# Kernel optimization log

Hardware: AMD Instinct MI355X
Metric: run time of the kernel (lower is better)

## Reference

```python
import jax, jax.numpy as jnp
import numpy as np

N, E, G = 50000, 800000, 16
NODE, HID, OUT, HEADS = 128, 64, 128, 3
NEG_SLOPE = 0.2

def setup_inputs() -> dict:
    key = jax.random.key(0)
    ks = jax.random.split(key, 12)
    h = jax.random.normal(ks[0], (N, NODE), jnp.float32)
    z = jax.random.normal(ks[1], (G, OUT), jnp.float32)
    src = jax.random.randint(ks[2], (E,), 0, N, jnp.int32)
    dst = jax.random.randint(ks[3], (E,), 0, N, jnp.int32)
    graph_id = jnp.sort(jax.random.randint(ks[4], (N,), 0, G, jnp.int32))
    s = 0.1
    fc_w = jax.random.normal(ks[5], (HEADS * HID, NODE), jnp.float32) * s
    attn_l = jax.random.normal(ks[6], (HEADS, HID), jnp.float32) * s
    attn_r = jax.random.normal(ks[7], (HEADS, HID), jnp.float32) * s
    bias = jnp.zeros((HEADS * HID,), jnp.float32)
    lin1_w = jax.random.normal(ks[8], (HID, OUT), jnp.float32) * s
    lin1_b = jnp.zeros((HID,), jnp.float32)
    lin2_w = jax.random.normal(ks[9], (1, 2 * HID), jnp.float32) * s
    lin2_b = jnp.zeros((1,), jnp.float32)
    return dict(h=h, z=z, src=src, dst=dst, graph_id=graph_id, fc_w=fc_w,
                attn_l=attn_l, attn_r=attn_r, bias=bias,
                lin1_w=lin1_w, lin1_b=lin1_b, lin2_w=lin2_w, lin2_b=lin2_b)

def reference(h, z, src, dst, graph_id, fc_w, attn_l, attn_r, bias,
              lin1_w, lin1_b, lin2_w, lin2_b):
    n = h.shape[0]
    # GATConv: projection -> [N, H, D]
    feat = (h @ fc_w.T).reshape(n, HEADS, HID)
    el = jnp.sum(feat * attn_l, axis=-1)  # [N, H]
    er = jnp.sum(feat * attn_r, axis=-1)  # [N, H]
    e = jax.nn.leaky_relu(el[src] + er[dst], NEG_SLOPE)  # [E, H]
    # edge softmax per destination node
    m = jax.ops.segment_max(e, dst, num_segments=n)
    e = jnp.exp(e - m[dst])
    s = jax.ops.segment_sum(e, dst, num_segments=n)
    alpha = e / s[dst]
    # scatter-weighted aggregation
    msg = alpha[:, :, None] * feat[src]  # [E, H, D]
    rst = jax.ops.segment_sum(msg, dst, num_segments=n)  # [N, H, D]
    rst = rst + bias.reshape(HEADS, HID)
    h_d = jnp.mean(rst, axis=1)  # [N, D] (mean over heads)
    # dgl.mean_nodes: per-graph mean pooling
    counts = jax.ops.segment_sum(jnp.ones((n,), h_d.dtype), graph_id, num_segments=G)
    pooled = jax.ops.segment_sum(h_d, graph_id, num_segments=G) / jnp.maximum(counts, 1.0)[:, None]
    z1 = z @ lin1_w.T + lin1_b  # [G, HID]
    cat = jnp.concatenate([pooled, z1], axis=1)  # [G, 2*HID]
    score = jax.nn.sigmoid(cat @ lin2_w.T + lin2_b)  # [G, 1]
    return score
```

## Files before the change

kernel.cpp:

```cpp
#include <hip/hip_runtime.h>
#include <math.h>

#define N_NODES 50000
#define N_EDGES 800000
#define N_GRAPHS 16
#define NODE_F 128
#define HID 64
#define OUT_F 128
#define HEADS 3
#define NEG 0.2f
#define FEAT (HEADS*HID)

typedef float f32x4 __attribute__((ext_vector_type(4)));
typedef float f32x2 __attribute__((ext_vector_type(2)));
typedef short bf16x8 __attribute__((ext_vector_type(8)));

#if defined(__has_builtin)
#if __has_builtin(__builtin_amdgcn_cvt_pk_f32_fp8) && __has_builtin(__builtin_amdgcn_cvt_pk_fp8_f32)
#define USE_FP8 1
#endif
#endif
#ifndef USE_FP8
#define USE_FP8 0
#endif

#if USE_FP8
#define FB 1
#else
#define FB 2
#endif
#define GRP (8 * FB)
#define ROW (32 * GRP)

#define DEG_PAD 32

__device__ __forceinline__ ushort f2bf(float x) {
  union { float f; unsigned u; } v; v.f = x;
  unsigned r = v.u + 0x7fff + ((v.u >> 16) & 1);
  return (ushort)(r >> 16);
}
__device__ __forceinline__ float bf2f(ushort x) {
  union { unsigned u; float f; } v; v.u = ((unsigned)x) << 16;
  return v.f;
}

__device__ __forceinline__ void feat_store(unsigned char* base, int n, int hh, int dd, float v) {
  size_t off = (size_t)n * ROW + (dd >> 1) * GRP + ((hh * 2 + (dd & 1)) * FB);
#if USE_FP8
  base[off] = (unsigned char)(__builtin_amdgcn_cvt_pk_fp8_f32(v, 0.f, 0, false) & 0xff);
#else
  *(ushort*)(base + off) = f2bf(v);
#endif
}

#define ZERO_INTS (N_GRAPHS * HID + N_GRAPHS + N_NODES * DEG_PAD)
#define ZERO_U4 (ZERO_INTS / 4)
#define ZB ((ZERO_U4 + 255) / 256)
__global__ void kprep(const float* __restrict__ fc_w, ushort* __restrict__ fcb,
                      uint4* __restrict__ zbase) {
  if (blockIdx.x >= 24) {
    int i = (blockIdx.x - 24) * 256 + threadIdx.x;
    if (i < ZERO_U4) zbase[i] = make_uint4(0, 0, 0, 0);
    return;
  }
  int i = blockIdx.x * 256 + threadIdx.x;
  int col = i >> 5;
  int kb = (i & 31) * 4;
  float4 v = *(const float4*)(fc_w + (size_t)col * NODE_F + kb);
  int t = col >> 4, m = col & 15;
  int kk = kb >> 5, kq = (kb >> 3) & 3, j = kb & 7;
  size_t idx0 = ((((size_t)t * 4 + kk) * 4 + kq) * 16 + m) * 8 + j;
  ushort4 o; o.x = f2bf(v.x); o.y = f2bf(v.y); o.z = f2bf(v.z); o.w = f2bf(v.w);
  *(ushort4*)(fcb + idx0) = o;
}

#define GB0 ((N_NODES + 63) / 64)
#define EB 5
#define HB2 (N_EDGES / (256 * EB))
__global__ __launch_bounds__(256) void k01_fused(
    const float* __restrict__ h, const ushort* __restrict__ fcb,
    const float* __restrict__ attn_l, const float* __restrict__ attn_r,
    const int* __restrict__ dst,
    unsigned char* __restrict__ feat, float* __restrict__ el, float* __restrict__ er,
    int* __restrict__ deg, int* __restrict__ rank)
{
  __shared__ ushort A[64][136];
  const int tid = threadIdx.x;

  if (blockIdx.x < HB2) {
    const int base = blockIdx.x * (256 * EB) + tid;
    int d[EB], r[EB];
#pragma unroll
    for (int i = 0; i < EB; i++) d[i] = dst[base + i * 256];
#pragma unroll
    for (int i = 0; i < EB; i++) r[i] = atomicAdd(&deg[d[i] * DEG_PAD], 1);
#pragma unroll
    for (int i = 0; i < EB; i++) rank[base + i * 256] = r[i];
    return;
  }

  const int n0 = (blockIdx.x - HB2) * 64;
  for (int i = tid; i < 64 * 32; i += 256) {
    int r = i >> 5, c4 = i & 31;
    if (n0 + r < N_NODES) {
      float4 v = *(const float4*)(h + (size_t)(n0 + r) * NODE_F + c4 * 4);
      unsigned lo = f2bf(v.x) | ((unsigned)f2bf(v.y) << 16);
      unsigned hi = f2bf(v.z) | ((unsigned)f2bf(v.w) << 16);
      *(uint2*)&A[r][c4 * 4] = make_uint2(lo, hi);
    }
  }
  __syncthreads();

  const int lane = tid & 63, wv = tid >> 6;
  const int m = lane & 15, kq = lane >> 4;

  f32x4 acc[12];
#pragma unroll
  for (int t = 0; t < 12; t++) acc[t] = (f32x4){0.f, 0.f, 0.f, 0.f};

#pragma unroll
  for (int kk = 0; kk < 4; kk++) {
    bf16x8 af = *(const bf16x8*)&A[wv * 16 + m][kk * 32 + kq * 8];
#pragma unroll
    for (int t = 0; t < 12; t++) {
      const bf16x8 bf = *(const bf16x8*)(fcb + ((((size_t)t * 4 + kk) * 4 + kq) * 16 + m) * 8);
      acc[t] = __builtin_amdgcn_mfma_f32_16x16x32_bf16(af, bf, acc[t], 0, 0, 0);
    }
  }

  const int rbase = n0 + wv * 16 + kq * 4;
#pragma unroll
  for (int t = 0; t < 12; t++) {
    const int hh = t >> 2;
    const int dd = (t & 3) * 16 + m;
#pragma unroll
    for (int reg = 0; reg < 4; reg++) {
      int n = rbase + reg;
      if (n < N_NODES) feat_store(feat, n, hh, dd, acc[t][reg]);
    }
  }

#pragma unroll
  for (int hh = 0; hh < HEADS; hh++) {
    float elv[4] = {0.f, 0.f, 0.f, 0.f};
    float erv[4] = {0.f, 0.f, 0.f, 0.f};
#pragma unroll
    for (int tt = 0; tt < 4; tt++) {
      int t = hh * 4 + tt;
      float al = attn_l[hh * HID + tt * 16 + m];
      float ar = attn_r[hh * HID + tt * 16 + m];
#pragma unroll
      for (int reg = 0; reg < 4; reg++) {
        elv[reg] = fmaf(acc[t][reg], al, elv[reg]);
        erv[reg] = fmaf(acc[t][reg], ar, erv[reg]);
      }
    }
#pragma unroll
    for (int reg = 0; reg < 4; reg++) {
#pragma unroll
      for (int off = 1; off < 16; off <<= 1) {
        elv[reg] += __shfl_xor(elv[reg], off, 64);
        erv[reg] += __shfl_xor(erv[reg], off, 64);
      }
      int n = rbase + reg;
      if (m == 0 && n < N_NODES) {
        el[(size_t)n * 4 + hh] = elv[reg];
        er[(size_t)n * 4 + hh] = erv[reg];
      }
    }
  }
}

#define SCAN_T 1024
#define SCAN_NB 49

__global__ __launch_bounds__(SCAN_T) void k2a_blocksum(
    const int* __restrict__ deg, int* __restrict__ bsum)
{
  const int tid = threadIdx.x;
  int idx = blockIdx.x * SCAN_T + tid;
  int v = (idx < N_NODES) ? deg[(size_t)idx * DEG_PAD] : 0;
#pragma unroll
  for (int off = 32; off; off >>= 1) v += __shfl_xor(v, off, 64);
  __shared__ int ws_[16];
  if ((tid & 63) == 0) ws_[tid >> 6] = v;
  __syncthreads();
  if (tid == 0) {
    int s = 0;
    for (int i = 0; i < 16; i++) s += ws_[i];
    bsum[blockIdx.x] = s;
  }
}

__global__ __launch_bounds__(SCAN_T) void k2c_apply(
    const int* __restrict__ deg, const int* __restrict__ bsum,
    int* __restrict__ offs)
{
  __shared__ int wsum[16], woff[16], bo;
  const int tid = threadIdx.x;
  const int lane = tid & 63, wv = tid >> 6;
  const int idx = blockIdx.x * SCAN_T + tid;
  if (tid < 64) {
    int v = (tid < blockIdx.x) ? bsum[tid] : 0;
#pragma unroll
    for (int off = 32; off; off >>= 1) v += __shfl_xor(v, off, 64);
    if (tid == 0) bo = v;
  }
  int v = (idx < N_NODES) ? deg[(size_t)idx * DEG_PAD] : 0;
  int s = v;
#pragma unroll
  for (int off = 1; off < 64; off <<= 1) {
    int t = __shfl_up(s, off, 64);
    if (lane >= off) s += t;
  }
  if (lane == 63) wsum[wv] = s;
  __syncthreads();
  if (tid < 16) {
    int w = wsum[tid];
    int sc = w;
#pragma unroll
    for (int off = 1; off < 16; off <<= 1) {
      int t = __shfl_up(sc, off, 64);
      if (tid >= off) sc += t;
    }
    woff[tid] = sc - w;
  }
  __syncthreads();
  int excl = s - v + woff[wv] + bo;
  if (idx < N_NODES) offs[idx] = excl;
  if (blockIdx.x == 0 && tid == 0) offs[N_NODES] = N_EDGES;
}

__global__ __launch_bounds__(256) void k3_edge(
    const int* __restrict__ src, const int* __restrict__ dst,
    const float* __restrict__ el4, const float* __restrict__ er4,
    const int* __restrict__ offs, const int* __restrict__ rank,
    float4* __restrict__ csr_w)
{
  int e = blockIdx.x * 256 + threadIdx.x;
  int s = src[e], d = dst[e];
  int pos = offs[d] + rank[e];
  float4 elv = ((const float4*)el4)[s];
  float4 erv = ((const float4*)er4)[d];
  float e0 = elv.x + erv.x; e0 = e0 > 0.f ? e0 : NEG * e0;
  float e1 = elv.y + erv.y; e1 = e1 > 0.f ? e1 : NEG * e1;
  float e2 = elv.z + erv.z; e2 = e2 > 0.f ? e2 : NEG * e2;
  float4 r;
  r.x = __expf(e0); r.y = __expf(e1); r.z = __expf(e2);
  r.w = __int_as_float(s * ROW);
  csr_w[pos] = r;
}

__global__ __launch_bounds__(256) void k4_agg(
    const int* __restrict__ offs, const float4* __restrict__ csr_w,
    const unsigned char* __restrict__ feat, const float* __restrict__ bias,
    float* __restrict__ h_d)
{
  __shared__ float4 rec[4][64];
  const int wv = threadIdx.x >> 6, lane = threadIdx.x & 63;
  const int n = blockIdx.x * 4 + wv;
  const int lo = offs[n], hi = offs[n + 1];
  const int half = lane >> 5;
  const int d = lane & 31;
  const char* fb = (const char*)feat;

  float a0x = 0.f, a0y = 0.f, a1x = 0.f, a1y = 0.f, a2x = 0.f, a2y = 0.f;
  float s0 = 0.f, s1 = 0.f, s2 = 0.f;

  for (int base = lo; base < hi; base += 64) {
    const int cnt = min(64, hi - base);
    if (lane < cnt) {
      float4 c = csr_w[base + lane];
      rec[wv][lane] = c;
      s0 += c.x; s1 += c.y; s2 += c.z;
    }
#define K4_BODY(J) do { \
      float4 c = rec[wv][J]; \
      const char* rp = fb + __float_as_int(c.w) + GRP * d; \
      f32x2 f0, f1, f2; \
      if (USE_FP8) { \
        uint2 q = *(const uint2*)rp; \
        f0 = __builtin_amdgcn_cvt_pk_f32_fp8(q.x & 0xffff, false); \
        f1 = __builtin_amdgcn_cvt_pk_f32_fp8(q.x >> 16, false); \
        f2 = __builtin_amdgcn_cvt_pk_f32_fp8(q.y & 0xffff, false); \
      } else { \
        uint4 q = *(const uint4*)rp; \
        f0.x = bf2f((ushort)(q.x & 0xffff)); f0.y = bf2f((ushort)(q.x >> 16)); \
        f1.x = bf2f((ushort)(q.y & 0xffff)); f1.y = bf2f((ushort)(q.y >> 16)); \
        f2.x = bf2f((ushort)(q.z & 0xffff)); f2.y = bf2f((ushort)(q.z >> 16)); \
      } \
      a0x = fmaf(c.x, f0.x, a0x); a0y = fmaf(c.x, f0.y, a0y); \
      a1x = fmaf(c.y, f1.x, a1x); a1y = fmaf(c.y, f1.y, a1y); \
      a2x = fmaf(c.z, f2.x, a2x); a2y = fmaf(c.z, f2.y, a2y); \
    } while (0)
    int j = half;
    for (; j + 2 < cnt; j += 4) { K4_BODY(j); K4_BODY(j + 2); }
    if (j < cnt) K4_BODY(j);
#undef K4_BODY
  }
  a0x += __shfl_xor(a0x, 32, 64); a0y += __shfl_xor(a0y, 32, 64);
  a1x += __shfl_xor(a1x, 32, 64); a1y += __shfl_xor(a1y, 32, 64);
  a2x += __shfl_xor(a2x, 32, 64); a2y += __shfl_xor(a2y, 32, 64);
#pragma unroll
  for (int off = 32; off; off >>= 1) {
    s0 += __shfl_xor(s0, off, 64);
    s1 += __shfl_xor(s1, off, 64);
    s2 += __shfl_xor(s2, off, 64);
  }
  const float i0 = s0 > 0.f ? 1.f / s0 : 0.f;
  const float i1 = s1 > 0.f ? 1.f / s1 : 0.f;
  const float i2 = s2 > 0.f ? 1.f / s2 : 0.f;
  if (half == 0) {
    float2 b0 = *(const float2*)(bias + 2 * d);
    float2 b1 = *(const float2*)(bias + HID + 2 * d);
    float2 b2 = *(const float2*)(bias + 2 * HID + 2 * d);
    float2 o;
    o.x = (fmaf(a0x, i0, b0.x) + fmaf(a1x, i1, b1.x) + fmaf(a2x, i2, b2.x)) * (1.f / 3.f);
    o.y = (fmaf(a0y, i0, b0.y) + fmaf(a1y, i1, b1.y) + fmaf(a2y, i2, b2.y)) * (1.f / 3.f);
    *(float2*)(h_d + (size_t)n * HID + 2 * d) = o;
  }
}

#define K5_NPB 128
#define K5_NB ((N_NODES + K5_NPB - 1) / K5_NPB)
#define NSEG (K5_NB * 2)
__global__ __launch_bounds__(256) void k5a_partial(
    const int* __restrict__ graph_id, const float* __restrict__ h_d,
    float* __restrict__ pooled_res, int* __restrict__ gcnt_res,
    float* __restrict__ part, int* __restrict__ pg, int* __restrict__ pc)
{
  const int wv = threadIdx.x >> 6, lane = threadIdx.x & 63;
  const int b = blockIdx.x;
  const int n0 = b * K5_NPB;
  const int n1 = min(n0 + K5_NPB, N_NODES);
  const int g_lo = graph_id[n0], g_hi = graph_id[n1 - 1];

  if (g_hi > g_lo + 1) {
    float acc = 0.f; int cur_g = -1; int cnt = 0;
    for (int i = n0 + wv; i < n1; i += 4) {
      int g = graph_id[i];
      if (g != cur_g) {
        if (cur_g >= 0) {
          atomicAdd(&pooled_res[cur_g * HID + lane], acc);
          if (lane == 0) atomicAdd(&gcnt_res[cur_g], cnt);
        }
        acc = 0.f; cnt = 0; cur_g = g;
      }
      acc += h_d[(size_t)i * HID + lane];
      cnt++;
    }
    if (cur_g >= 0) {
      atomicAdd(&pooled_res[cur_g * HID + lane], acc);
      if (lane == 0) atomicAdd(&gcnt_res[cur_g], cnt);
    }
    if (threadIdx.x < 2) pg[b * 2 + threadIdx.x] = -1;
    return;
  }

  float acc_lo = 0.f, acc_hi = 0.f;
  int c_lo = 0, c_hi = 0;
  for (int i = n0 + wv; i < n1; i += 4) {
    int g = graph_id[i];
    float v = h_d[(size_t)i * HID + lane];
    bool hi = (g != g_lo);
    acc_hi += hi ? v : 0.f;
    acc_lo += hi ? 0.f : v;
    c_hi += hi ? 1 : 0;
    c_lo += hi ? 0 : 1;
  }
  __shared__ float ls[2][4][64];
  __shared__ int lc[2][4];
  ls[0][wv][lane] = acc_lo;
  ls[1][wv][lane] = acc_hi;
  if (lane == 0) { lc[0][wv] = c_lo; lc[1][wv] = c_hi; }
  __syncthreads();
  if (wv < 2) {
    float s = ls[wv][0][lane] + ls[wv][1][lane] + ls[wv][2][lane] + ls[wv][3][lane];
    part[((size_t)b * 2 + wv) * HID + lane] = s;
    if (lane == 0) {
      int cnt = lc[wv][0] + lc[wv][1] + lc[wv][2] + lc[wv][3];
      int gg = (wv == 0) ? g_lo : g_hi;
      if (wv == 1 && (g_hi == g_lo || cnt == 0)) gg = -1;
      pg[b * 2 + wv] = gg;
      pc[b * 2 + wv] = cnt;
    }
  }
}

__global__ __launch_bounds__(256) void k6_final(
    const float* __restrict__ part, const int* __restrict__ pg, const int* __restrict__ pc,
    const float* __restrict__ pooled_res, const int* __restrict__ gcnt_res,
    const float* __restrict__ z,
    const float* __restrict__ lin1_w, const float* __restrict__ lin1_b,
    const float* __restrict__ lin2_w, const float* __restrict__ lin2_b,
    float* __restrict__ out)
{
  const int g = blockIdx.x;
  const int tid = threadIdx.x, wv = tid >> 6, lane = tid & 63;
  __shared__ int spg[NSEG], spc[NSEG];
  __shared__ float red[4][HID];
  __shared__ int rc[4];
  __shared__ float cat[2 * HID];

  for (int i = tid; i < NSEG; i += 256) { spg[i] = pg[i]; spc[i] = pc[i]; }
  __syncthreads();

  float acc = 0.f; int cnt = 0;
  for (int s = wv; s < NSEG; s += 4) {
    if (spg[s] == g) {
      acc += part[(size_t)s * HID + lane];
      cnt += spc[s];
    }
  }
  red[wv][lane] = acc;
  if (lane == 0) rc[wv] = cnt;
  __syncthreads();

  if (wv == 0) {
    float s = red[0][lane] + red[1][lane] + red[2][lane] + red[3][lane]
            + pooled_res[g * HID + lane];
    int c = rc[0] + rc[1] + rc[2] + rc[3] + gcnt_res[g];
    cat[lane] = s / (float)(c > 0 ? c : 1);
  }
  if (wv == 1) {
    float s = lin1_b[lane];
    const float* zr = z + g * OUT_F;
    const float* wr = lin1_w + lane * OUT_F;
    for (int k = 0; k < OUT_F; k += 4) {
      float4 zv = *(const float4*)(zr + k);
      float4 wv4 = *(const float4*)(wr + k);
      s = fmaf(zv.x, wv4.x, fmaf(zv.y, wv4.y, fmaf(zv.z, wv4.z, fmaf(zv.w, wv4.w, s))));
    }
    cat[HID + lane] = s;
  }
  __syncthreads();
  if (wv == 0) {
    float s = cat[lane] * lin2_w[lane] + cat[HID + lane] * lin2_w[HID + lane];
#pragma unroll
    for (int off = 32; off; off >>= 1) s += __shfl_xor(s, off, 64);
    if (lane == 0) out[g] = 1.f / (1.f + __expf(-(s + lin2_b[0])));
  }
}

extern "C" void kernel_launch(void* const* d_in, const int* in_sizes, int n_in,
                              void* d_out, int out_size, void* d_ws, size_t ws_size,
                              hipStream_t stream) {
  (void)in_sizes; (void)n_in; (void)out_size; (void)ws_size;
  const float* h      = (const float*)d_in[0];
  const float* z      = (const float*)d_in[1];
  const int*   src    = (const int*)d_in[2];
  const int*   dst    = (const int*)d_in[3];
  const int*   gid    = (const int*)d_in[4];
  const float* fc_w   = (const float*)d_in[5];
  const float* attn_l = (const float*)d_in[6];
  const float* attn_r = (const float*)d_in[7];
  const float* bias   = (const float*)d_in[8];
  const float* lin1_w = (const float*)d_in[9];
  const float* lin1_b = (const float*)d_in[10];
  const float* lin2_w = (const float*)d_in[11];
  const float* lin2_b = (const float*)d_in[12];
  float* out = (float*)d_out;

  float4* csr_w     = (float4*)d_ws;
  unsigned char* feat = (unsigned char*)(csr_w + N_EDGES);
  float* h_d        = (float*)(feat + (size_t)N_NODES * ROW);
  float* el         = h_d + (size_t)N_NODES * HID;
  float* er         = el + (size_t)N_NODES * 4;
  float* part       = er + (size_t)N_NODES * 4;
  int* pg           = (int*)(part + (size_t)NSEG * HID);
  int* pc           = pg + NSEG;
  ushort* fcb       = (ushort*)(pc + NSEG);
  float* pooled_res = (float*)(fcb + 192 * NODE_F);
  int* gcnt_res     = (int*)(pooled_res + N_GRAPHS * HID);
  int* deg          = gcnt_res + N_GRAPHS;
  int* offs         = deg + (size_t)N_NODES * DEG_PAD;
  int* rank         = offs + (N_NODES + 1);
  int* bsum         = rank + N_EDGES;

  kprep<<<24 + ZB, 256, 0, stream>>>(fc_w, fcb, (uint4*)pooled_res);
  k01_fused<<<HB2 + GB0, 256, 0, stream>>>(h, fcb, attn_l, attn_r, dst,
                                           feat, el, er, deg, rank);
  k2a_blocksum<<<SCAN_NB, SCAN_T, 0, stream>>>(deg, bsum);
  k2c_apply<<<SCAN_NB, SCAN_T, 0, stream>>>(deg, bsum, offs);
  k3_edge<<<N_EDGES / 256, 256, 0, stream>>>(src, dst, el, er, offs, rank, csr_w);
  k4_agg<<<N_NODES / 4, 256, 0, stream>>>(offs, csr_w, feat, bias, h_d);
  k5a_partial<<<K5_NB, 256, 0, stream>>>(gid, h_d, pooled_res, gcnt_res, part, pg, pc);
  k6_final<<<N_GRAPHS, 256, 0, stream>>>(part, pg, pc, pooled_res, gcnt_res,
                                         z, lin1_w, lin1_b, lin2_w, lin2_b, out);
}
```

Before: 229.5 us.

## Replace global-atomic CSR build with two-level bucketed counting sort

Replaces the per-edge global atomic degree counting (with padded counters) and two-kernel scan with a two-pass bucketed counting sort. Edges are first histogrammed into 64-node buckets with shared-memory atomics, then scanned and scattered into buckets, and finally sorted per node within each bucket. This removes contended global atomics and the padded degree array, and lets k3_edge read sorted (src,dst) pairs and write output contiguously. In exchange it adds more kernel launches, an extra pass over the edges, and no longer overlaps the GEMM with the degree counting.

```diff
diff --git a/kernel.cpp b/kernel.cpp
--- a/kernel.cpp
+++ b/kernel.cpp
@@ -32,7 +32,9 @@
 #define GRP (8 * FB)
 #define ROW (32 * GRP)
 
-#define DEG_PAD 32
+#define NBKT ((N_NODES + 63) / 64)
+#define H1B 400
+#define EPB (N_EDGES / H1B)
 
 __device__ __forceinline__ ushort f2bf(float x) {
   union { float f; unsigned u; } v; v.f = x;
@@ -53,7 +55,7 @@
 #endif
 }
 
-#define ZERO_INTS (N_GRAPHS * HID + N_GRAPHS + N_NODES * DEG_PAD)
+#define ZERO_INTS (N_GRAPHS * HID + N_GRAPHS)
 #define ZERO_U4 (ZERO_INTS / 4)
 #define ZB ((ZERO_U4 + 255) / 256)
 __global__ void kprep(const float* __restrict__ fc_w, ushort* __restrict__ fcb,
@@ -75,31 +77,15 @@
 }
 
 #define GB0 ((N_NODES + 63) / 64)
-#define EB 5
-#define HB2 (N_EDGES / (256 * EB))
-__global__ __launch_bounds__(256) void k01_fused(
+__global__ __launch_bounds__(256) void k1_gemm(
     const float* __restrict__ h, const ushort* __restrict__ fcb,
     const float* __restrict__ attn_l, const float* __restrict__ attn_r,
-    const int* __restrict__ dst,
-    unsigned char* __restrict__ feat, float* __restrict__ el, float* __restrict__ er,
-    int* __restrict__ deg, int* __restrict__ rank)
+    unsigned char* __restrict__ feat, float* __restrict__ el, float* __restrict__ er)
 {
   __shared__ ushort A[64][136];
   const int tid = threadIdx.x;
 
-  if (blockIdx.x < HB2) {
-    const int base = blockIdx.x * (256 * EB) + tid;
-    int d[EB], r[EB];
-#pragma unroll
-    for (int i = 0; i < EB; i++) d[i] = dst[base + i * 256];
-#pragma unroll
-    for (int i = 0; i < EB; i++) r[i] = atomicAdd(&deg[d[i] * DEG_PAD], 1);
-#pragma unroll
-    for (int i = 0; i < EB; i++) rank[base + i * 256] = r[i];
-    return;
-  }
-
-  const int n0 = (blockIdx.x - HB2) * 64;
+  const int n0 = blockIdx.x * 64;
   for (int i = tid; i < 64 * 32; i += 256) {
     int r = i >> 5, c4 = i & 31;
     if (n0 + r < N_NODES) {
@@ -171,75 +157,141 @@
   }
 }
 
-#define SCAN_T 1024
-#define SCAN_NB 49
-
-__global__ __launch_bounds__(SCAN_T) void k2a_blocksum(
-    const int* __restrict__ deg, int* __restrict__ bsum)
-{
-  const int tid = threadIdx.x;
-  int idx = blockIdx.x * SCAN_T + tid;
-  int v = (idx < N_NODES) ? deg[(size_t)idx * DEG_PAD] : 0;
-#pragma unroll
-  for (int off = 32; off; off >>= 1) v += __shfl_xor(v, off, 64);
-  __shared__ int ws_[16];
-  if ((tid & 63) == 0) ws_[tid >> 6] = v;
-  __syncthreads();
-  if (tid == 0) {
-    int s = 0;
-    for (int i = 0; i < 16; i++) s += ws_[i];
-    bsum[blockIdx.x] = s;
-  }
-}
-
-__global__ __launch_bounds__(SCAN_T) void k2c_apply(
-    const int* __restrict__ deg, const int* __restrict__ bsum,
-    int* __restrict__ offs)
-{
-  __shared__ int wsum[16], woff[16], bo;
-  const int tid = threadIdx.x;
-  const int lane = tid & 63, wv = tid >> 6;
-  const int idx = blockIdx.x * SCAN_T + tid;
-  if (tid < 64) {
-    int v = (tid < blockIdx.x) ? bsum[tid] : 0;
-#pragma unroll
-    for (int off = 32; off; off >>= 1) v += __shfl_xor(v, off, 64);
-    if (tid == 0) bo = v;
-  }
-  int v = (idx < N_NODES) ? deg[(size_t)idx * DEG_PAD] : 0;
-  int s = v;
+__global__ __launch_bounds__(256) void kh1_hist(
+    const int* __restrict__ dst, int* __restrict__ cnt_g)
+{
+  __shared__ int cnt[NBKT];
+  const int tid = threadIdx.x, blk = blockIdx.x;
+  for (int i = tid; i < NBKT; i += 256) cnt[i] = 0;
+  __syncthreads();
+  const int e0 = blk * EPB;
+  for (int i = tid; i < EPB; i += 256)
+    atomicAdd(&cnt[dst[e0 + i] >> 6], 1);
+  __syncthreads();
+  for (int i = tid; i < NBKT; i += 256) cnt_g[(size_t)blk * NBKT + i] = cnt[i];
+}
+
+#define H2A_K 7
+__global__ __launch_bounds__(64) void kh2a_scan(
+    const int* __restrict__ cnt_g, int* __restrict__ base_bm, int* __restrict__ btot)
+{
+  const int b = blockIdx.x;
+  const int lane = threadIdx.x;
+  int v[H2A_K];
+  int lt = 0;
+#pragma unroll
+  for (int j = 0; j < H2A_K; j++) {
+    int g = lane * H2A_K + j;
+    v[j] = (g < H1B) ? cnt_g[(size_t)g * NBKT + b] : 0;
+    lt += v[j];
+  }
+  int s = lt;
 #pragma unroll
   for (int off = 1; off < 64; off <<= 1) {
     int t = __shfl_up(s, off, 64);
     if (lane >= off) s += t;
   }
-  if (lane == 63) wsum[wv] = s;
-  __syncthreads();
-  if (tid < 16) {
-    int w = wsum[tid];
-    int sc = w;
-#pragma unroll
-    for (int off = 1; off < 16; off <<= 1) {
-      int t = __shfl_up(sc, off, 64);
-      if (tid >= off) sc += t;
-    }
-    woff[tid] = sc - w;
-  }
-  __syncthreads();
-  int excl = s - v + woff[wv] + bo;
-  if (idx < N_NODES) offs[idx] = excl;
-  if (blockIdx.x == 0 && tid == 0) offs[N_NODES] = N_EDGES;
+  int excl = s - lt;
+#pragma unroll
+  for (int j = 0; j < H2A_K; j++) {
+    int g = lane * H2A_K + j;
+    if (g < H1B) base_bm[(size_t)b * H1B + g] = excl;
+    excl += v[j];
+  }
+  if (lane == 63) btot[b] = s;
+}
+
+#define H2B_K 13
+__global__ __launch_bounds__(64) void kh2b_scan(
+    const int* __restrict__ btot, int* __restrict__ bucket_off)
+{
+  const int lane = threadIdx.x;
+  int v[H2B_K];
+  int lt = 0;
+#pragma unroll
+  for (int j = 0; j < H2B_K; j++) {
+    int g = lane * H2B_K + j;
+    v[j] = (g < NBKT) ? btot[g] : 0;
+    lt += v[j];
+  }
+  int s = lt;
+#pragma unroll
+  for (int off = 1; off < 64; off <<= 1) {
+    int t = __shfl_up(s, off, 64);
+    if (lane >= off) s += t;
+  }
+  int excl = s - lt;
+#pragma unroll
+  for (int j = 0; j < H2B_K; j++) {
+    int g = lane * H2B_K + j;
+    if (g < NBKT) bucket_off[g] = excl;
+    excl += v[j];
+  }
+  if (lane == 63) bucket_off[NBKT] = s;
+}
+
+__global__ __launch_bounds__(256) void kh3_scatter(
+    const int* __restrict__ src, const int* __restrict__ dst,
+    const int* __restrict__ bucket_off, const int* __restrict__ base_bm,
+    int2* __restrict__ pairs)
+{
+  __shared__ int cur[NBKT];
+  const int tid = threadIdx.x, blk = blockIdx.x;
+  for (int i = tid; i < NBKT; i += 256)
+    cur[i] = bucket_off[i] + base_bm[(size_t)i * H1B + blk];
+  __syncthreads();
+  const int e0 = blk * EPB;
+  for (int i = tid; i < EPB; i += 256) {
+    int e = e0 + i;
+    int d = dst[e], s = src[e];
+    int slot = atomicAdd(&cur[d >> 6], 1);
+    pairs[slot] = make_int2(s, d);
+  }
+}
+
+__global__ __launch_bounds__(256) void kh4_nodesort(
+    const int2* __restrict__ pairs, const int* __restrict__ bucket_off,
+    int2* __restrict__ pairs_s, int* __restrict__ offs)
+{
+  __shared__ int nodecnt[64];
+  __shared__ int cur[64];
+  const int b = blockIdx.x, tid = threadIdx.x;
+  const int lo = bucket_off[b], hi = bucket_off[b + 1];
+  if (tid < 64) nodecnt[tid] = 0;
+  __syncthreads();
+  for (int i = lo + tid; i < hi; i += 256)
+    atomicAdd(&nodecnt[pairs[i].y & 63], 1);
+  __syncthreads();
+  if (tid < 64) {
+    int v = nodecnt[tid];
+    int s = v;
+#pragma unroll
+    for (int off = 1; off < 64; off <<= 1) {
+      int t = __shfl_up(s, off, 64);
+      if (tid >= off) s += t;
+    }
+    int excl = s - v;
+    cur[tid] = lo + excl;
+    int n = b * 64 + tid;
+    if (n < N_NODES) offs[n] = lo + excl;
+    if (b == NBKT - 1 && tid == 0) offs[N_NODES] = hi;
+  }
+  __syncthreads();
+  for (int i = lo + tid; i < hi; i += 256) {
+    int2 pr = pairs[i];
+    int slot = atomicAdd(&cur[pr.y & 63], 1);
+    pairs_s[slot] = pr;
+  }
 }
 
 __global__ __launch_bounds__(256) void k3_edge(
-    const int* __restrict__ src, const int* __restrict__ dst,
+    const int2* __restrict__ pairs_s,
     const float* __restrict__ el4, const float* __restrict__ er4,
-    const int* __restrict__ offs, const int* __restrict__ rank,
     float4* __restrict__ csr_w)
 {
   int e = blockIdx.x * 256 + threadIdx.x;
-  int s = src[e], d = dst[e];
-  int pos = offs[d] + rank[e];
+  int2 pr = pairs_s[e];
+  int s = pr.x, d = pr.y;
   float4 elv = ((const float4*)el4)[s];
   float4 erv = ((const float4*)er4)[d];
   float e0 = elv.x + erv.x; e0 = e0 > 0.f ? e0 : NEG * e0;
@@ -248,7 +300,7 @@
   float4 r;
   r.x = __expf(e0); r.y = __expf(e1); r.z = __expf(e2);
   r.w = __int_as_float(s * ROW);
-  csr_w[pos] = r;
+  csr_w[e] = r;
 }
 
 __global__ __launch_bounds__(256) void k4_agg(
@@ -462,6 +514,7 @@
   float* out = (float*)d_out;
 
   float4* csr_w     = (float4*)d_ws;
+  int2* pairs       = (int2*)csr_w;
   unsigned char* feat = (unsigned char*)(csr_w + N_EDGES);
   float* h_d        = (float*)(feat + (size_t)N_NODES * ROW);
   float* el         = h_d + (size_t)N_NODES * HID;
@@ -472,17 +525,21 @@
   ushort* fcb       = (ushort*)(pc + NSEG);
   float* pooled_res = (float*)(fcb + 192 * NODE_F);
   int* gcnt_res     = (int*)(pooled_res + N_GRAPHS * HID);
-  int* deg          = gcnt_res + N_GRAPHS;
-  int* offs         = deg + (size_t)N_NODES * DEG_PAD;
-  int* rank         = offs + (N_NODES + 1);
-  int* bsum         = rank + N_EDGES;
+  int* offs         = gcnt_res + N_GRAPHS;
+  int2* pairs_s     = (int2*)(offs + (N_NODES + 1));
+  int* cnt_g        = (int*)(pairs_s + N_EDGES);
+  int* base_bm      = cnt_g + (size_t)H1B * NBKT;
+  int* btot         = base_bm + (size_t)NBKT * H1B;
+  int* bucket_off   = btot + NBKT;
 
   kprep<<<24 + ZB, 256, 0, stream>>>(fc_w, fcb, (uint4*)pooled_res);
-  k01_fused<<<HB2 + GB0, 256, 0, stream>>>(h, fcb, attn_l, attn_r, dst,
-                                           feat, el, er, deg, rank);
-  k2a_blocksum<<<SCAN_NB, SCAN_T, 0, stream>>>(deg, bsum);
-  k2c_apply<<<SCAN_NB, SCAN_T, 0, stream>>>(deg, bsum, offs);
-  k3_edge<<<N_EDGES / 256, 256, 0, stream>>>(src, dst, el, er, offs, rank, csr_w);
+  k1_gemm<<<GB0, 256, 0, stream>>>(h, fcb, attn_l, attn_r, feat, el, er);
+  kh1_hist<<<H1B, 256, 0, stream>>>(dst, cnt_g);
+  kh2a_scan<<<NBKT, 64, 0, stream>>>(cnt_g, base_bm, btot);
+  kh2b_scan<<<1, 64, 0, stream>>>(btot, bucket_off);
+  kh3_scatter<<<H1B, 256, 0, stream>>>(src, dst, bucket_off, base_bm, pairs);
+  kh4_nodesort<<<NBKT, 256, 0, stream>>>(pairs, bucket_off, pairs_s, offs);
+  k3_edge<<<N_EDGES / 256, 256, 0, stream>>>(pairs_s, el, er, csr_w);
   k4_agg<<<N_NODES / 4, 256, 0, stream>>>(offs, csr_w, feat, bias, h_d);
   k5a_partial<<<K5_NB, 256, 0, stream>>>(gid, h_d, pooled_res, gcnt_res, part, pg, pc);
   k6_final<<<N_GRAPHS, 256, 0, stream>>>(part, pg, pc, pooled_res, gcnt_res,
```

Measured after the change: 217.1 us. 1.06x faster.
